# Kernel tuning notes

Measured on AMD Instinct MI355X. Metric: run time of the kernel, lower is better.

## Reference

```python
import jax, jax.numpy as jnp
import numpy as np

B = 4096
IN = 1723 * 6          # 10338
H = 1024
OUT = 24 * 3 * 3 + 10 + 3  # 229
EPS = 1e-5


def _bn(x, g, b):
    # BatchNorm1d training-mode forward: biased batch statistics
    mu = jnp.mean(x, axis=0)
    var = jnp.var(x, axis=0)
    return g * (x - mu) * jax.lax.rsqrt(var + EPS) + b


def _resblock(h, wa, ba, ga, bea, wb, bb, gb, beb):
    t = jax.nn.relu(_bn(h @ wa + ba, ga, bea))
    t = _bn(t @ wb + bb, gb, beb)
    return jax.nn.relu(h + t)


def setup_inputs() -> dict:
    key = jax.random.key(0)
    ks = jax.random.split(key, 16)
    s = 0.02
    inp = {"x": jax.random.normal(ks[0], (B, IN), dtype=jnp.float32)}
    # FCBlock(IN -> H): Linear + BN + ReLU
    inp["w1"] = jax.random.normal(ks[1], (IN, H), dtype=jnp.float32) * s
    inp["b1"] = jnp.zeros((H,), jnp.float32)
    inp["g1"] = jnp.ones((H,), jnp.float32)
    inp["be1"] = jnp.zeros((H,), jnp.float32)
    # two FCResBlocks (H -> H)
    for i, kk in zip((2, 3), (ks[2:4], ks[4:6])):
        inp[f"w{i}a"] = jax.random.normal(kk[0], (H, H), dtype=jnp.float32) * s
        inp[f"b{i}a"] = jnp.zeros((H,), jnp.float32)
        inp[f"g{i}a"] = jnp.ones((H,), jnp.float32)
        inp[f"be{i}a"] = jnp.zeros((H,), jnp.float32)
        inp[f"w{i}b"] = jax.random.normal(kk[1], (H, H), dtype=jnp.float32) * s
        inp[f"b{i}b"] = jnp.zeros((H,), jnp.float32)
        inp[f"g{i}b"] = jnp.ones((H,), jnp.float32)
        inp[f"be{i}b"] = jnp.zeros((H,), jnp.float32)
    # final Linear (H -> OUT)
    inp["w4"] = jax.random.normal(ks[6], (H, OUT), dtype=jnp.float32) * s
    inp["b4"] = jnp.zeros((OUT,), jnp.float32)
    return inp


def reference(x, w1, b1, g1, be1,
              w2a, b2a, g2a, be2a, w2b, b2b, g2b, be2b,
              w3a, b3a, g3a, be3a, w3b, b3b, g3b, be3b,
              w4, b4):
    batch = x.shape[0]
    h = jax.nn.relu(_bn(x @ w1 + b1, g1, be1))
    h = _resblock(h, w2a, b2a, g2a, be2a, w2b, b2b, g2b, be2b)
    h = _resblock(h, w3a, b3a, g3a, be3a, w3b, b3b, g3b, be3b)
    out = h @ w4 + b4                              # (B, 229)

    rotmat = out[:, :216].reshape(-1, 3, 3)        # (B*24, 3, 3)
    betas = out[:, 216:226]                        # (B, 10)
    camera = out[:, 226:]                          # (B, 3)

    # batched 3x3 SVD orthogonalization (replaces per-sample Python loop)
    U, S, Vh = jnp.linalg.svd(rotmat, full_matrices=False)
    R = U @ Vh
    # det computed under no_grad in original -> stop_gradient
    det = jax.lax.stop_gradient(jnp.linalg.det(R))[:, None, None]
    R = (R * det).reshape(batch, 24, 3, 3)
    return (R, betas, camera)
```

## Files before the change

### kernel.cpp

```cpp
#include <hip/hip_runtime.h>
#include <math.h>


typedef _Float16 half8 __attribute__((ext_vector_type(8)));
typedef _Float16 half4_t __attribute__((ext_vector_type(4)));
typedef float floatx4 __attribute__((ext_vector_type(4)));

#define LO_SCALE 4096.0f
#define LO_INV (1.0f / 4096.0f)
#define IN_C 10338
#define INP_C 10368

__device__ __forceinline__ void gld16(const _Float16* g, _Float16* l) {
  __builtin_amdgcn_global_load_lds(
      (const __attribute__((address_space(1))) void*)g,
      (__attribute__((address_space(3))) void*)l, 16, 0, 0);
}

template <int TAG>
__global__ __launch_bounds__(256, 2)
void gemm_sk(const _Float16* __restrict__ Ah, const _Float16* __restrict__ Al,
             const _Float16* __restrict__ Bh, const _Float16* __restrict__ Bl,
             float* __restrict__ Cp, int Kld, int Ncols, int Ks,
             size_t partStride) {
  __shared__ _Float16 sAh[2][4096], sAl[2][4096];
  __shared__ _Float16 sBh[2][4096], sBl[2][4096];
  const int tid = threadIdx.x;
  const int wv = tid >> 6, ln = tid & 63;
  const int ln15 = ln & 15, q = ln >> 4;
  const int wr = wv >> 1, wc = wv & 1;
  const int bm0 = blockIdx.x * 128, bn0 = blockIdx.y * 128;
  const int k0 = blockIdx.z * Ks;
  Cp += (size_t)blockIdx.z * partStride;

  const int srow = ln >> 2;
  const int swzw = (ln & 3) ^ (srow & 3) ^ ((srow >> 2) & 3);
  const int ch0 = wv * 2, ch1 = wv * 2 + 1;
  const size_t offA0 = (size_t)(bm0 + ch0 * 16 + srow) * Kld + k0 + swzw * 8;
  const size_t offA1 = (size_t)(bm0 + ch1 * 16 + srow) * Kld + k0 + swzw * 8;
  const size_t offB0 = (size_t)(bn0 + ch0 * 16 + srow) * Kld + k0 + swzw * 8;
  const size_t offB1 = (size_t)(bn0 + ch1 * 16 + srow) * Kld + k0 + swzw * 8;

  const int swzr = (q ^ (ln15 & 3) ^ ((ln15 >> 2) & 3)) * 8;
  const int aoff = (wr * 64 + ln15) * 32 + swzr;
  const int boff = (wc * 64 + ln15) * 32 + swzr;

  floatx4 acc[4][4];
  floatx4 acc2[4][4];
#pragma unroll
  for (int i = 0; i < 4; ++i)
#pragma unroll
    for (int j = 0; j < 4; ++j) {
      acc[i][j] = (floatx4){0.f, 0.f, 0.f, 0.f};
      acc2[i][j] = (floatx4){0.f, 0.f, 0.f, 0.f};
    }

  auto stage = [&](int kt, int buf) {
    gld16(Ah + offA0 + kt, &sAh[buf][ch0 * 512]);
    gld16(Ah + offA1 + kt, &sAh[buf][ch1 * 512]);
    gld16(Al + offA0 + kt, &sAl[buf][ch0 * 512]);
    gld16(Al + offA1 + kt, &sAl[buf][ch1 * 512]);
    gld16(Bh + offB0 + kt, &sBh[buf][ch0 * 512]);
    gld16(Bh + offB1 + kt, &sBh[buf][ch1 * 512]);
    gld16(Bl + offB0 + kt, &sBl[buf][ch0 * 512]);
    gld16(Bl + offB1 + kt, &sBl[buf][ch1 * 512]);
  };

  stage(0, 0);
  int cur = 0;
  for (int kt = 0; kt < Ks; kt += 32) {
    __syncthreads();
    if (kt + 32 < Ks) stage(kt + 32, cur ^ 1);

    const _Float16* pAh = &sAh[cur][aoff];
    const _Float16* pAl = &sAl[cur][aoff];
    const _Float16* pBh = &sBh[cur][boff];
    const _Float16* pBl = &sBl[cur][boff];
    half8 bh[4], bl[4];
#pragma unroll
    for (int ni = 0; ni < 4; ++ni) {
      bh[ni] = *(const half8*)(pBh + ni * 512);
      bl[ni] = *(const half8*)(pBl + ni * 512);
    }
#pragma unroll
    for (int mh = 0; mh < 2; ++mh) {
      half8 ah[2], al[2];
#pragma unroll
      for (int i = 0; i < 2; ++i) {
        ah[i] = *(const half8*)(pAh + (mh * 2 + i) * 512);
        al[i] = *(const half8*)(pAl + (mh * 2 + i) * 512);
      }
#pragma unroll
      for (int i = 0; i < 2; ++i) {
        const int mi = mh * 2 + i;
#pragma unroll
        for (int ni = 0; ni < 4; ++ni) {
          acc[mi][ni] = __builtin_amdgcn_mfma_f32_16x16x32_f16(
              ah[i], bh[ni], acc[mi][ni], 0, 0, 0);
          acc2[mi][ni] = __builtin_amdgcn_mfma_f32_16x16x32_f16(
              ah[i], bl[ni], acc2[mi][ni], 0, 0, 0);
          acc2[mi][ni] = __builtin_amdgcn_mfma_f32_16x16x32_f16(
              al[i], bh[ni], acc2[mi][ni], 0, 0, 0);
        }
      }
    }
    cur ^= 1;
  }

#pragma unroll
  for (int mi = 0; mi < 4; ++mi)
#pragma unroll
    for (int ni = 0; ni < 4; ++ni) {
      const int col = bn0 + wc * 64 + ni * 16 + ln15;
      const int rbase = bm0 + wr * 64 + mi * 16 + q * 4;
#pragma unroll
      for (int r = 0; r < 4; ++r)
        Cp[(size_t)(rbase + r) * Ncols + col] =
            acc[mi][ni][r] + acc2[mi][ni][r] * LO_INV;
    }
}

__global__ __launch_bounds__(256)
void split_pad_v(const float* __restrict__ X, _Float16* __restrict__ xh,
                 _Float16* __restrict__ xl, int total8) {
  int di = blockIdx.x * 256 + threadIdx.x;
  if (di >= total8) return;
  int base = di * 8;
  int row = base / INP_C;
  int col0 = base - row * INP_C;
  const float* src = X + (size_t)row * IN_C + col0;
  float v[8];
#pragma unroll
  for (int j = 0; j < 8; ++j) v[j] = (col0 + j < IN_C) ? src[j] : 0.f;
  half8 h, l;
#pragma unroll
  for (int j = 0; j < 8; ++j) {
    _Float16 hh = (_Float16)v[j];
    h[j] = hh;
    l[j] = (_Float16)((v[j] - (float)hh) * LO_SCALE);
  }
  *(half8*)(xh + base) = h;
  *(half8*)(xl + base) = l;
}

struct TJob {
  const float* src;
  _Float16* th;
  _Float16* tl;
  int K, N, Kpad, tK, start;
};
struct TJobs {
  TJob j[6];
};

__global__ __launch_bounds__(256)
void transpose_all(TJobs J) {
  const int b = blockIdx.x;
  int ji = 0;
#pragma unroll
  for (int i = 1; i < 6; ++i)
    if (b >= J.j[i].start) ji = i;
  const TJob job = J.j[ji];
  const int t = b - job.start;
  const int kk0 = (t % job.tK) * 32;
  const int nn0 = (t / job.tK) * 32;

  __shared__ float ts[32][33];
  const int tid = threadIdx.x;
  const int tx = tid & 31, ty = tid >> 5;
#pragma unroll
  for (int r = 0; r < 4; ++r) {
    int kk = kk0 + ty + r * 8;
    int nn = nn0 + tx;
    ts[ty + r * 8][tx] =
        (kk < job.K && nn < job.N) ? job.src[(size_t)kk * job.N + nn] : 0.f;
  }
  __syncthreads();
  const int tw = tid & 7, rw = tid >> 3;
  const int nn = nn0 + rw, kk = kk0 + tw * 4;
  half4_t h, l;
#pragma unroll
  for (int i2 = 0; i2 < 4; ++i2) {
    float v = ts[tw * 4 + i2][rw];
    _Float16 hh = (_Float16)v;
    h[i2] = hh;
    l[i2] = (_Float16)((v - (float)hh) * LO_SCALE);
  }
  size_t o = (size_t)nn * job.Kpad + kk;
  *(half4_t*)(job.th + o) = h;
  *(half4_t*)(job.tl + o) = l;
}

__global__ __launch_bounds__(256)
void reduce_bias_stats_v(const float* __restrict__ Cp,
                         const float* __restrict__ bias, float* __restrict__ Y,
                         float* __restrict__ psum, float* __restrict__ psq,
                         int S, size_t stride, int rowsPer) {
  const int N = 1024;
  const int t = threadIdx.x;
  const int cg = t & 63, rl = t >> 6;
  const int col4 = blockIdx.x * 256 + cg * 4;
  const int r0 = blockIdx.y * rowsPer;
  const floatx4 bs = *(const floatx4*)(bias + col4);
  floatx4 s = {0.f, 0.f, 0.f, 0.f}, qq = {0.f, 0.f, 0.f, 0.f};
  for (int r = r0 + rl; r < r0 + rowsPer; r += 4) {
    size_t i = (size_t)r * N + col4;
    floatx4 v = bs;
    for (int k = 0; k < S; ++k) v += *(const floatx4*)(Cp + k * stride + i);
    *(floatx4*)(Y + i) = v;
    s += v;
    qq += v * v;
  }
  __shared__ floatx4 ls[4][64], lq[4][64];
  ls[rl][cg] = s;
  lq[rl][cg] = qq;
  __syncthreads();
  if (t < 64) {
    floatx4 S4 = ls[0][t] + ls[1][t] + ls[2][t] + ls[3][t];
    floatx4 Q4 = lq[0][t] + lq[1][t] + lq[2][t] + lq[3][t];
    size_t o = (size_t)blockIdx.y * N + blockIdx.x * 256 + t * 4;
    *(floatx4*)(psum + o) = S4;
    *(floatx4*)(psq + o) = Q4;
  }
}

__global__ __launch_bounds__(256)
void bn_apply_v(const float* __restrict__ Y, const float* __restrict__ psum,
                const float* __restrict__ psq, const float* __restrict__ g,
                const float* __restrict__ be, const float* __restrict__ res,
                float* __restrict__ outf, _Float16* __restrict__ oh,
                _Float16* __restrict__ ol, int RB, float invM) {
  const int N = 1024;
  const int t = threadIdx.x;
  const int cg = t & 63, rl = t >> 6;
  const int col4 = blockIdx.x * 256 + cg * 4;
  __shared__ floatx4 lA[64], lB[64];
  if (t < 64) {
    int c4 = blockIdx.x * 256 + t * 4;
    floatx4 s = {0.f, 0.f, 0.f, 0.f}, qq = {0.f, 0.f, 0.f, 0.f};
    for (int rb = 0; rb < RB; ++rb) {
      s += *(const floatx4*)(psum + (size_t)rb * N + c4);
      qq += *(const floatx4*)(psq + (size_t)rb * N + c4);
    }
    floatx4 m = s * invM;
    floatx4 var = qq * invM - m * m;
    floatx4 rstd;
#pragma unroll
    for (int i = 0; i < 4; ++i) rstd[i] = rsqrtf(var[i] + 1e-5f);
    floatx4 a = (*(const floatx4*)(g + c4)) * rstd;
    lA[t] = a;
    lB[t] = (*(const floatx4*)(be + c4)) - m * a;
  }
  __syncthreads();
  const floatx4 a = lA[cg], b2 = lB[cg];
#pragma unroll
  for (int rr = 0; rr < 2; ++rr) {
    const int r = blockIdx.y * 8 + rl + rr * 4;
    const size_t i = (size_t)r * N + col4;
    floatx4 v = (*(const floatx4*)(Y + i)) * a + b2;
    if (res) v += *(const floatx4*)(res + i);
#pragma unroll
    for (int ii = 0; ii < 4; ++ii) v[ii] = fmaxf(v[ii], 0.f);
    if (outf) *(floatx4*)(outf + i) = v;
    half4_t h, l;
#pragma unroll
    for (int ii = 0; ii < 4; ++ii) {
      _Float16 hh = (_Float16)v[ii];
      h[ii] = hh;
      l[ii] = (_Float16)((v[ii] - (float)hh) * LO_SCALE);
    }
    *(half4_t*)(oh + i) = h;
    *(half4_t*)(ol + i) = l;
  }
}

__global__ void reduce_bias_head_v(const float* __restrict__ Cp,
                                   const float* __restrict__ bias,
                                   float* __restrict__ Y, int total4, int S,
                                   size_t stride) {
  int i4 = blockIdx.x * 256 + threadIdx.x;
  if (i4 >= total4) return;
  size_t i = (size_t)i4 * 4;
  int c = (int)(i & 255);
  floatx4 v = {0.f, 0.f, 0.f, 0.f};
  for (int k = 0; k < S; ++k) v += *(const floatx4*)(Cp + k * stride + i);
#pragma unroll
  for (int j = 0; j < 4; ++j) {
    int cc = c + j;
    v[j] += (cc < 229) ? bias[cc] : 0.f;
  }
  *(floatx4*)(Y + i) = v;
}

__device__ __forceinline__ void cofactor3(const float X[9], float C[9]) {
  C[0] = X[4] * X[8] - X[5] * X[7];
  C[1] = X[5] * X[6] - X[3] * X[8];
  C[2] = X[3] * X[7] - X[4] * X[6];
  C[3] = X[2] * X[7] - X[1] * X[8];
  C[4] = X[0] * X[8] - X[2] * X[6];
  C[5] = X[1] * X[6] - X[0] * X[7];
  C[6] = X[1] * X[5] - X[2] * X[4];
  C[7] = X[2] * X[3] - X[0] * X[5];
  C[8] = X[0] * X[4] - X[1] * X[3];
}

__global__ __launch_bounds__(256)
void polar_tail(const float* __restrict__ Y, float* __restrict__ out, int Bt,
                int nmat, int ldy) {
  int idx = blockIdx.x * blockDim.x + threadIdx.x;
  if (idx < nmat) {
    int s = idx / 24, j = idx % 24;
    const float* a = Y + (size_t)s * ldy + j * 9;
    float A[9], X[9];
#pragma unroll
    for (int k = 0; k < 9; ++k) {
      A[k] = a[k];
      X[k] = A[k];
    }
    double detA = (double)A[0] * ((double)A[4] * A[8] - (double)A[5] * A[7]) -
                  (double)A[1] * ((double)A[3] * A[8] - (double)A[5] * A[6]) +
                  (double)A[2] * ((double)A[3] * A[7] - (double)A[4] * A[6]);
    float sgn = (detA < 0.0) ? -1.f : 1.f;
#pragma unroll 1
    for (int it = 0; it < 12; ++it) {
      float C[9];
      cofactor3(X, C);
      float det = X[0] * C[0] + X[1] * C[1] + X[2] * C[2];
      float ad = fmaxf(fabsf(det), 1e-30f);
      float idet = (det < 0.f ? -1.f : 1.f) / ad;
      float n1 = 0.f, n2 = 0.f;
#pragma unroll
      for (int k = 0; k < 9; ++k) {
        n1 += X[k] * X[k];
        n2 += C[k] * C[k];
      }
      n1 = fmaxf(n1, 1e-30f);
      float zeta = sqrtf(sqrtf(n2 * idet * idet / n1));
      zeta = fminf(fmaxf(zeta, 1e-4f), 1e4f);
      float iz = 0.5f / zeta;
      float hz = 0.5f * zeta;
#pragma unroll
      for (int k = 0; k < 9; ++k) X[k] = hz * X[k] + iz * idet * C[k];
    }
    float* o = out + (size_t)idx * 9;
#pragma unroll
    for (int k = 0; k < 9; ++k) o[k] = X[k] * sgn;
  } else {
    int i = idx - nmat;
    int nb = Bt * 10;
    int nc = Bt * 3;
    if (i < nb) {
      int s = i / 10, k = i % 10;
      out[(size_t)Bt * 216 + i] = Y[(size_t)s * ldy + 216 + k];
    } else if (i < nb + nc) {
      int t = i - nb;
      int s = t / 3, k = t % 3;
      out[(size_t)Bt * 216 + nb + t] = Y[(size_t)s * ldy + 226 + k];
    }
  }
}

extern "C" void kernel_launch(void* const* d_in, const int* in_sizes, int n_in,
                              void* d_out, int out_size, void* d_ws,
                              size_t ws_size, hipStream_t stream) {
  const float* x = (const float*)d_in[0];
  const float* w1 = (const float*)d_in[1];
  const float* b1 = (const float*)d_in[2];
  const float* g1 = (const float*)d_in[3];
  const float* be1 = (const float*)d_in[4];
  const float* w2a = (const float*)d_in[5];
  const float* b2a = (const float*)d_in[6];
  const float* g2a = (const float*)d_in[7];
  const float* be2a = (const float*)d_in[8];
  const float* w2b = (const float*)d_in[9];
  const float* b2b = (const float*)d_in[10];
  const float* g2b = (const float*)d_in[11];
  const float* be2b = (const float*)d_in[12];
  const float* w3a = (const float*)d_in[13];
  const float* b3a = (const float*)d_in[14];
  const float* g3a = (const float*)d_in[15];
  const float* be3a = (const float*)d_in[16];
  const float* w3b = (const float*)d_in[17];
  const float* b3b = (const float*)d_in[18];
  const float* g3b = (const float*)d_in[19];
  const float* be3b = (const float*)d_in[20];
  const float* w4 = (const float*)d_in[21];
  const float* b4 = (const float*)d_in[22];
  float* out = (float*)d_out;

  const int B = 4096, IN = 10338, INP = 10368, H = 1024;
  const int OUTN = 229, OUTP = 256;
  const int RB = 32;
  const int S_BIG = 2, S_MID = 2, S_HEAD = 8;

  char* p = (char*)d_ws;
  auto alloc = [&](size_t bytes) -> void* {
    void* r = (void*)p;
    p += (bytes + 255) & ~(size_t)255;
    return r;
  };
  float* Cpart = (float*)alloc((size_t)S_HEAD * B * OUTP * 4);
  float* Y = (float*)alloc((size_t)B * H * 4);
  float* Hf = (float*)alloc((size_t)B * H * 4);
  _Float16* xh = (_Float16*)alloc((size_t)B * INP * 2);
  _Float16* xl = (_Float16*)alloc((size_t)B * INP * 2);
  _Float16* w1h = (_Float16*)alloc((size_t)H * INP * 2);
  _Float16* w1l = (_Float16*)alloc((size_t)H * INP * 2);
  _Float16 *wmh[4], *wml[4];
  for (int i = 0; i < 4; ++i) {
    wmh[i] = (_Float16*)alloc((size_t)H * H * 2);
    wml[i] = (_Float16*)alloc((size_t)H * H * 2);
  }
  _Float16* w4h = (_Float16*)alloc((size_t)OUTP * H * 2);
  _Float16* w4l = (_Float16*)alloc((size_t)OUTP * H * 2);
  _Float16* hh = (_Float16*)alloc((size_t)B * H * 2);
  _Float16* hl = (_Float16*)alloc((size_t)B * H * 2);
  float* psum = (float*)alloc((size_t)RB * H * 4);
  float* psq = (float*)alloc((size_t)RB * H * 4);

  {
    int total8 = B * INP / 8;
    split_pad_v<<<dim3((total8 + 255) / 256), 256, 0, stream>>>(x, xh, xl,
                                                                total8);
    TJobs J;
    const float* wsrc[6] = {w1, w2a, w2b, w3a, w3b, w4};
    _Float16* th[6] = {w1h, wmh[0], wmh[1], wmh[2], wmh[3], w4h};
    _Float16* tl[6] = {w1l, wml[0], wml[1], wml[2], wml[3], w4l};
    int Ks[6] = {IN, H, H, H, H, H};
    int Ns[6] = {H, H, H, H, H, OUTN};
    int Kpads[6] = {INP, H, H, H, H, H};
    int Npads[6] = {H, H, H, H, H, OUTP};
    int start = 0;
    for (int i = 0; i < 6; ++i) {
      J.j[i].src = wsrc[i];
      J.j[i].th = th[i];
      J.j[i].tl = tl[i];
      J.j[i].K = Ks[i];
      J.j[i].N = Ns[i];
      J.j[i].Kpad = Kpads[i];
      J.j[i].tK = Kpads[i] / 32;
      J.j[i].start = start;
      start += (Kpads[i] / 32) * (Npads[i] / 32);
    }
    transpose_all<<<dim3(start), 256, 0, stream>>>(J);
  }

  auto reducestats = [&](const float* bias, int S) {
    reduce_bias_stats_v<<<dim3(H / 256, RB), 256, 0, stream>>>(
        Cpart, bias, Y, psum, psq, S, (size_t)B * H, B / RB);
  };
  auto bnapply = [&](const float* g, const float* be, const float* res,
                     float* outf) {
    bn_apply_v<<<dim3(H / 256, B / 8), 256, 0, stream>>>(
        Y, psum, psq, g, be, res, outf, hh, hl, RB, 1.f / B);
  };

  gemm_sk<0><<<dim3(B / 128, H / 128, S_BIG), 256, 0, stream>>>(
      xh, xl, w1h, w1l, Cpart, INP, H, INP / S_BIG, (size_t)B * H);
  reducestats(b1, S_BIG);
  bnapply(g1, be1, nullptr, Hf);
  gemm_sk<1><<<dim3(B / 128, H / 128, S_MID), 256, 0, stream>>>(
      hh, hl, wmh[0], wml[0], Cpart, H, H, H / S_MID, (size_t)B * H);
  reducestats(b2a, S_MID);
  bnapply(g2a, be2a, nullptr, nullptr);
  gemm_sk<1><<<dim3(B / 128, H / 128, S_MID), 256, 0, stream>>>(
      hh, hl, wmh[1], wml[1], Cpart, H, H, H / S_MID, (size_t)B * H);
  reducestats(b2b, S_MID);
  bnapply(g2b, be2b, Hf, Hf);
  gemm_sk<1><<<dim3(B / 128, H / 128, S_MID), 256, 0, stream>>>(
      hh, hl, wmh[2], wml[2], Cpart, H, H, H / S_MID, (size_t)B * H);
  reducestats(b3a, S_MID);
  bnapply(g3a, be3a, nullptr, nullptr);
  gemm_sk<1><<<dim3(B / 128, H / 128, S_MID), 256, 0, stream>>>(
      hh, hl, wmh[3], wml[3], Cpart, H, H, H / S_MID, (size_t)B * H);
  reducestats(b3b, S_MID);
  bnapply(g3b, be3b, Hf, Hf);
  gemm_sk<2><<<dim3(B / 128, OUTP / 128, S_HEAD), 256, 0, stream>>>(
      hh, hl, w4h, w4l, Cpart, H, OUTP, H / S_HEAD, (size_t)B * OUTP);
  {
    int total4 = B * OUTP / 4;
    reduce_bias_head_v<<<dim3((total4 + 255) / 256), 256, 0, stream>>>(
        Cpart, b4, Y, total4, S_HEAD, (size_t)B * OUTP);
  }

  int nmat = B * 24;
  int ntot = nmat + B * 13;
  polar_tail<<<dim3((ntot + 255) / 256), 256, 0, stream>>>(Y, out, B, nmat,
                                                           OUTP);
}
```

Before: 1.001 ms.

## Remap GEMM grid to 1D swizzle, widen stats reduction grid, fuse head reduce into polar

```diff
diff --git a/kernel.cpp b/kernel.cpp
--- a/kernel.cpp
+++ b/kernel.cpp
@@ -17,7 +17,7 @@
       (__attribute__((address_space(3))) void*)l, 16, 0, 0);
 }
 
-template <int TAG>
+template <int TAG, int NY>
 __global__ __launch_bounds__(256, 2)
 void gemm_sk(const _Float16* __restrict__ Ah, const _Float16* __restrict__ Al,
              const _Float16* __restrict__ Bh, const _Float16* __restrict__ Bl,
@@ -29,9 +29,15 @@
   const int wv = tid >> 6, ln = tid & 63;
   const int ln15 = ln & 15, q = ln >> 4;
   const int wr = wv >> 1, wc = wv & 1;
-  const int bm0 = blockIdx.x * 128, bn0 = blockIdx.y * 128;
-  const int k0 = blockIdx.z * Ks;
-  Cp += (size_t)blockIdx.z * partStride;
+
+  const int gid = blockIdx.x;
+  const int slot = gid >> 3;
+  const int yz = (gid & 7) + 8 * (slot & 1);
+  const int bm0 = (slot >> 1) * 128;
+  const int bn0 = (yz % NY) * 128;
+  const int bz = yz / NY;
+  const int k0 = bz * Ks;
+  Cp += (size_t)bz * partStride;
 
   const int srow = ln >> 2;
   const int swzw = (ln & 3) ^ (srow & 3) ^ ((srow >> 2) & 3);
@@ -198,12 +204,12 @@
                          int S, size_t stride, int rowsPer) {
   const int N = 1024;
   const int t = threadIdx.x;
-  const int cg = t & 63, rl = t >> 6;
-  const int col4 = blockIdx.x * 256 + cg * 4;
+  const int cg = t & 15, rl = t >> 4;
+  const int col4 = blockIdx.x * 64 + cg * 4;
   const int r0 = blockIdx.y * rowsPer;
   const floatx4 bs = *(const floatx4*)(bias + col4);
   floatx4 s = {0.f, 0.f, 0.f, 0.f}, qq = {0.f, 0.f, 0.f, 0.f};
-  for (int r = r0 + rl; r < r0 + rowsPer; r += 4) {
+  for (int r = r0 + rl; r < r0 + rowsPer; r += 16) {
     size_t i = (size_t)r * N + col4;
     floatx4 v = bs;
     for (int k = 0; k < S; ++k) v += *(const floatx4*)(Cp + k * stride + i);
@@ -211,14 +217,18 @@
     s += v;
     qq += v * v;
   }
-  __shared__ floatx4 ls[4][64], lq[4][64];
+  __shared__ floatx4 ls[16][16], lq[16][16];
   ls[rl][cg] = s;
   lq[rl][cg] = qq;
   __syncthreads();
-  if (t < 64) {
-    floatx4 S4 = ls[0][t] + ls[1][t] + ls[2][t] + ls[3][t];
-    floatx4 Q4 = lq[0][t] + lq[1][t] + lq[2][t] + lq[3][t];
-    size_t o = (size_t)blockIdx.y * N + blockIdx.x * 256 + t * 4;
+  if (t < 16) {
+    floatx4 S4 = {0.f, 0.f, 0.f, 0.f}, Q4 = {0.f, 0.f, 0.f, 0.f};
+#pragma unroll
+    for (int r = 0; r < 16; ++r) {
+      S4 += ls[r][t];
+      Q4 += lq[r][t];
+    }
+    size_t o = (size_t)blockIdx.y * N + blockIdx.x * 64 + t * 4;
     *(floatx4*)(psum + o) = S4;
     *(floatx4*)(psq + o) = Q4;
   }
@@ -274,24 +284,6 @@
   }
 }
 
-__global__ void reduce_bias_head_v(const float* __restrict__ Cp,
-                                   const float* __restrict__ bias,
-                                   float* __restrict__ Y, int total4, int S,
-                                   size_t stride) {
-  int i4 = blockIdx.x * 256 + threadIdx.x;
-  if (i4 >= total4) return;
-  size_t i = (size_t)i4 * 4;
-  int c = (int)(i & 255);
-  floatx4 v = {0.f, 0.f, 0.f, 0.f};
-  for (int k = 0; k < S; ++k) v += *(const floatx4*)(Cp + k * stride + i);
-#pragma unroll
-  for (int j = 0; j < 4; ++j) {
-    int cc = c + j;
-    v[j] += (cc < 229) ? bias[cc] : 0.f;
-  }
-  *(floatx4*)(Y + i) = v;
-}
-
 __device__ __forceinline__ void cofactor3(const float X[9], float C[9]) {
   C[0] = X[4] * X[8] - X[5] * X[7];
   C[1] = X[5] * X[6] - X[3] * X[8];
@@ -305,17 +297,21 @@
 }
 
 __global__ __launch_bounds__(256)
-void polar_tail(const float* __restrict__ Y, float* __restrict__ out, int Bt,
-                int nmat, int ldy) {
+void polar_tail(const float* __restrict__ Cp, const float* __restrict__ bias,
+                float* __restrict__ out, int Bt, int nmat, int S,
+                size_t stride) {
+  const int ldy = 256;
   int idx = blockIdx.x * blockDim.x + threadIdx.x;
   if (idx < nmat) {
     int s = idx / 24, j = idx % 24;
-    const float* a = Y + (size_t)s * ldy + j * 9;
+    const size_t base = (size_t)s * ldy + j * 9;
     float A[9], X[9];
 #pragma unroll
     for (int k = 0; k < 9; ++k) {
-      A[k] = a[k];
-      X[k] = A[k];
+      float v = bias[j * 9 + k];
+      for (int z = 0; z < S; ++z) v += Cp[z * stride + base + k];
+      A[k] = v;
+      X[k] = v;
     }
     double detA = (double)A[0] * ((double)A[4] * A[8] - (double)A[5] * A[7]) -
                   (double)A[1] * ((double)A[3] * A[8] - (double)A[5] * A[6]) +
@@ -349,14 +345,23 @@
     int i = idx - nmat;
     int nb = Bt * 10;
     int nc = Bt * 3;
+    int s, k, c;
     if (i < nb) {
-      int s = i / 10, k = i % 10;
-      out[(size_t)Bt * 216 + i] = Y[(size_t)s * ldy + 216 + k];
+      s = i / 10;
+      k = i;
+      c = 216 + (i % 10);
     } else if (i < nb + nc) {
-      int t = i - nb;
-      int s = t / 3, k = t % 3;
-      out[(size_t)Bt * 216 + nb + t] = Y[(size_t)s * ldy + 226 + k];
-    }
+      int t2 = i - nb;
+      s = t2 / 3;
+      k = i;
+      c = 226 + (t2 % 3);
+    } else {
+      return;
+    }
+    float v = bias[c];
+    size_t base = (size_t)s * ldy + c;
+    for (int z = 0; z < S; ++z) v += Cp[z * stride + base];
+    out[(size_t)Bt * 216 + k] = v;
   }
 }
 
@@ -446,7 +451,7 @@
   }
 
   auto reducestats = [&](const float* bias, int S) {
-    reduce_bias_stats_v<<<dim3(H / 256, RB), 256, 0, stream>>>(
+    reduce_bias_stats_v<<<dim3(16, RB), 256, 0, stream>>>(
         Cpart, bias, Y, psum, psq, S, (size_t)B * H, B / RB);
   };
   auto bnapply = [&](const float* g, const float* be, const float* res,
@@ -455,36 +460,32 @@
         Y, psum, psq, g, be, res, outf, hh, hl, RB, 1.f / B);
   };
 
-  gemm_sk<0><<<dim3(B / 128, H / 128, S_BIG), 256, 0, stream>>>(
-      xh, xl, w1h, w1l, Cpart, INP, H, INP / S_BIG, (size_t)B * H);
+  gemm_sk<0, 8><<<dim3(512), 256, 0, stream>>>(xh, xl, w1h, w1l, Cpart, INP, H,
+                                               INP / S_BIG, (size_t)B * H);
   reducestats(b1, S_BIG);
   bnapply(g1, be1, nullptr, Hf);
-  gemm_sk<1><<<dim3(B / 128, H / 128, S_MID), 256, 0, stream>>>(
-      hh, hl, wmh[0], wml[0], Cpart, H, H, H / S_MID, (size_t)B * H);
+  gemm_sk<1, 8><<<dim3(512), 256, 0, stream>>>(hh, hl, wmh[0], wml[0], Cpart,
+                                               H, H, H / S_MID, (size_t)B * H);
   reducestats(b2a, S_MID);
   bnapply(g2a, be2a, nullptr, nullptr);
-  gemm_sk<1><<<dim3(B / 128, H / 128, S_MID), 256, 0, stream>>>(
-      hh, hl, wmh[1], wml[1], Cpart, H, H, H / S_MID, (size_t)B * H);
+  gemm_sk<1, 8><<<dim3(512), 256, 0, stream>>>(hh, hl, wmh[1], wml[1], Cpart,
+                                               H, H, H / S_MID, (size_t)B * H);
   reducestats(b2b, S_MID);
   bnapply(g2b, be2b, Hf, Hf);
-  gemm_sk<1><<<dim3(B / 128, H / 128, S_MID), 256, 0, stream>>>(
-      hh, hl, wmh[2], wml[2], Cpart, H, H, H / S_MID, (size_t)B * H);
+  gemm_sk<1, 8><<<dim3(512), 256, 0, stream>>>(hh, hl, wmh[2], wml[2], Cpart,
+                                               H, H, H / S_MID, (size_t)B * H);
   reducestats(b3a, S_MID);
   bnapply(g3a, be3a, nullptr, nullptr);
-  gemm_sk<1><<<dim3(B / 128, H / 128, S_MID), 256, 0, stream>>>(
-      hh, hl, wmh[3], wml[3], Cpart, H, H, H / S_MID, (size_t)B * H);
+  gemm_sk<1, 8><<<dim3(512), 256, 0, stream>>>(hh, hl, wmh[3], wml[3], Cpart,
+                                               H, H, H / S_MID, (size_t)B * H);
   reducestats(b3b, S_MID);
   bnapply(g3b, be3b, Hf, Hf);
-  gemm_sk<2><<<dim3(B / 128, OUTP / 128, S_HEAD), 256, 0, stream>>>(
-      hh, hl, w4h, w4l, Cpart, H, OUTP, H / S_HEAD, (size_t)B * OUTP);
-  {
-    int total4 = B * OUTP / 4;
-    reduce_bias_head_v<<<dim3((total4 + 255) / 256), 256, 0, stream>>>(
-        Cpart, b4, Y, total4, S_HEAD, (size_t)B * OUTP);
-  }
+  gemm_sk<2, 2><<<dim3(512), 256, 0, stream>>>(hh, hl, w4h, w4l, Cpart, H,
+                                               OUTP, H / S_HEAD,
+                                               (size_t)B * OUTP);
 
   int nmat = B * 24;
   int ntot = nmat + B * 13;
-  polar_tail<<<dim3((ntot + 255) / 256), 256, 0, stream>>>(Y, out, B, nmat,
-                                                           OUTP);
-}
+  polar_tail<<<dim3((ntot + 255) / 256), 256, 0, stream>>>(
+      Cpart, b4, out, B, nmat, S_HEAD, (size_t)B * OUTP);
+}
```

Result: faster. 956.5 us (-4.5%).
